# Kernel optimization log

Measured on AMD Instinct MI355X. Metric: run time of the kernel, lower is better.

Reference implementation:

```python
import jax, jax.numpy as jnp
import numpy as np


def _chamfer_min_sqdist(a, b):
    # a: [N,3], b: [M,3] -> for each point in a, min squared distance to b. [N]
    # ||a||^2 + ||b||^2 - 2 a.b^T ; clamp tiny negatives from cancellation.
    a2 = jnp.sum(a * a, axis=-1)            # [N]
    b2 = jnp.sum(b * b, axis=-1)            # [M]
    cross = a @ b.T                          # [N,M] GEMM, K=3
    d = a2[:, None] + b2[None, :] - 2.0 * cross
    return jnp.maximum(jnp.min(d, axis=1), 0.0)


def setup_inputs() -> dict:
    key = jax.random.key(0)
    k1, k2 = jax.random.split(key)
    N = 16384
    state_x = jax.random.normal(k1, (N, 3), dtype=jnp.float32)
    target = jax.random.normal(k2, (N, 3), dtype=jnp.float32)
    return {"state_x": state_x, "target": target}


def reference(state_x, target):
    # dist1: target -> nearest in state_x ; dist2: state_x -> nearest in target
    dist1 = _chamfer_min_sqdist(target, state_x)   # [N]
    dist2 = _chamfer_min_sqdist(state_x, target)   # [N]
    loss = (jnp.mean(jnp.sqrt(dist1)) + jnp.mean(jnp.sqrt(dist2))) * 0.5
    return loss * 10.0
```

## Files before the change

kernel.cpp:

```cpp
#include <hip/hip_runtime.h>
#include <math.h>


typedef __attribute__((ext_vector_type(8)))  short bf16x8;
typedef __attribute__((ext_vector_type(16))) float f32x16;

#define S_SLICES 16

__device__ __forceinline__ unsigned enc_f32(float f) {
    int b = __float_as_int(f);
    return (b >= 0) ? ((unsigned)b | 0x80000000u) : ~(unsigned)b;
}
__device__ __forceinline__ float dec_f32(unsigned k) {
    int b = (k & 0x80000000u) ? (int)(k & 0x7FFFFFFFu) : ~(int)k;
    return __int_as_float(b);
}

__device__ __forceinline__ unsigned short f2bf(float v) {
    unsigned u = __float_as_uint(v);
    u += 0x7FFFu + ((u >> 16) & 1u);
    return (unsigned short)(u >> 16);
}
__device__ __forceinline__ float bf2f(unsigned short b) {
    unsigned u = ((unsigned)b) << 16;
    return __uint_as_float(u);
}
__device__ __forceinline__ unsigned pk2(unsigned short lo, unsigned short hi) {
    return (unsigned)lo | ((unsigned)hi << 16);
}

__global__ __launch_bounds__(256) void chamfer_prep(
    const float* __restrict__ state_x, const float* __restrict__ target,
    uint4* __restrict__ AfragS, uint4* __restrict__ AfragT,
    uint4* __restrict__ BfragS, uint4* __restrict__ BfragT,
    unsigned* __restrict__ mins_u, float* __restrict__ out, int N)
{
    const int p = blockIdx.x * 256 + threadIdx.x;
    const float* src = (p < N) ? state_x : target;
    const int i = (p < N) ? p : p - N;

    const float x = src[3*i+0], y = src[3*i+1], z = src[3*i+2];
    const float n2 = fmaf(x, x, fmaf(y, y, z * z));

    const unsigned short hx = f2bf(x), hy = f2bf(y), hz = f2bf(z);
    const unsigned short lx = f2bf(x - bf2f(hx));
    const unsigned short ly = f2bf(y - bf2f(hy));
    const unsigned short lz = f2bf(z - bf2f(hz));
    const unsigned short mhx = f2bf(-2.0f*x), mhy = f2bf(-2.0f*y), mhz = f2bf(-2.0f*z);
    const unsigned short mlx = f2bf(-2.0f*x - bf2f(mhx));
    const unsigned short mly = f2bf(-2.0f*y - bf2f(mhy));
    const unsigned short mlz = f2bf(-2.0f*z - bf2f(mhz));
    const unsigned short hn = f2bf(n2);
    const unsigned short ln = f2bf(n2 - bf2f(hn));
    const unsigned short ONE = 0x3F80;

    uint4 A0 = make_uint4(pk2(mhx,mhy), pk2(mhz,mlx), pk2(mly,mlz), pk2(mhx,mhy));
    uint4 A1 = make_uint4(pk2(mhz,mlx), pk2(mly,mlz), pk2(hn,ln),   pk2(ONE,ONE));
    uint4 B0 = make_uint4(pk2(hx,hy), pk2(hz,hx), pk2(hy,hz), pk2(lx,ly));
    uint4 B1 = make_uint4(pk2(lz,lx), pk2(ly,lz), pk2(ONE,ONE), pk2(hn,ln));

    uint4* Aarr = (p < N) ? AfragS : AfragT;
    uint4* Barr = (p < N) ? BfragS : BfragT;
    Aarr[2*i+0] = A0;  Aarr[2*i+1] = A1;
    Barr[2*i+0] = B0;  Barr[2*i+1] = B1;

    mins_u[p] = 0xFFFFFFFFu;
    if (p == 0) *out = 0.0f;
}

__global__ __launch_bounds__(256) void chamfer_main(
    const bf16x8* __restrict__ AfragS, const bf16x8* __restrict__ AfragT,
    const bf16x8* __restrict__ BfragS, const bf16x8* __restrict__ BfragT,
    unsigned* __restrict__ mins_u, int N, int S)
{
    const int tid  = threadIdx.x;
    const int lane = tid & 63;
    const int l31  = lane & 31;
    const int half = lane >> 5;
    const int w    = tid >> 6;

    const int bs = blockIdx.x / S;
    const int s  = blockIdx.x % S;
    const int qblk = bs * 256;

    const bf16x8* afr;
    const bf16x8* bfr;
    if (qblk < N) { afr = AfragT + (size_t)qblk * 2;       bfr = BfragS; }
    else          { afr = AfragS + (size_t)(qblk - N) * 2; bfr = BfragT; }

    const int C = N / S;

    __shared__ uint4 ldsB[2048];
    {
        const uint4* src = (const uint4*)bfr + (size_t)(s * C) * 2;
        #pragma unroll
        for (int j = 0; j < 8; ++j)
            ldsB[tid + j * 256] = src[tid + j * 256];
    }
    __syncthreads();
    const bf16x8* lb = (const bf16x8*)ldsB;

    const int r0 = w * 64;
    const bf16x8 av0 = afr[(r0 +      l31) * 2 + half];
    const bf16x8 av1 = afr[(r0 + 32 + l31) * 2 + half];

    const int boff = l31 * 2 + half;

    f32x16 racc0, racc1, zc;
    #pragma unroll
    for (int i = 0; i < 16; ++i) { racc0[i] = 3.0e38f; racc1[i] = 3.0e38f; zc[i] = 0.0f; }

    #pragma unroll 2
    for (int it = 0; it < C / 64; ++it) {
        const bf16x8 b0 = lb[it * 128 + boff];
        const bf16x8 b1 = lb[it * 128 + 64 + boff];
        {
            f32x16 a0 = __builtin_amdgcn_mfma_f32_32x32x16_bf16(av0, b0, zc, 0, 0, 0);
            f32x16 a1 = __builtin_amdgcn_mfma_f32_32x32x16_bf16(av0, b1, zc, 0, 0, 0);
            #pragma unroll
            for (int i = 0; i < 16; ++i)
                racc0[i] = fminf(fminf(racc0[i], a0[i]), a1[i]);
        }
        {
            f32x16 a0 = __builtin_amdgcn_mfma_f32_32x32x16_bf16(av1, b0, zc, 0, 0, 0);
            f32x16 a1 = __builtin_amdgcn_mfma_f32_32x32x16_bf16(av1, b1, zc, 0, 0, 0);
            #pragma unroll
            for (int i = 0; i < 16; ++i)
                racc1[i] = fminf(fminf(racc1[i], a0[i]), a1[i]);
        }
    }

    #pragma unroll
    for (int i = 0; i < 16; ++i) {
        float v0 = racc0[i], v1 = racc1[i];
        v0 = fminf(v0, __shfl_xor(v0, 16, 64));
        v1 = fminf(v1, __shfl_xor(v1, 16, 64));
        v0 = fminf(v0, __shfl_xor(v0,  8, 64));
        v1 = fminf(v1, __shfl_xor(v1,  8, 64));
        v0 = fminf(v0, __shfl_xor(v0,  4, 64));
        v1 = fminf(v1, __shfl_xor(v1,  4, 64));
        v0 = fminf(v0, __shfl_xor(v0,  2, 64));
        v1 = fminf(v1, __shfl_xor(v1,  2, 64));
        v0 = fminf(v0, __shfl_xor(v0,  1, 64));
        v1 = fminf(v1, __shfl_xor(v1,  1, 64));
        racc0[i] = v0;
        racc1[i] = v1;
    }

    if (l31 == 0) {
        const int base = qblk + r0;
        #pragma unroll
        for (int i = 0; i < 16; ++i) {
            const int row = (i & 3) + 8 * (i >> 2) + 4 * half;
            atomicMin(&mins_u[base + row],      enc_f32(racc0[i]));
            atomicMin(&mins_u[base + 32 + row], enc_f32(racc1[i]));
        }
    }
}

__global__ __launch_bounds__(256) void chamfer_finish(
    const unsigned* __restrict__ mins_u, float* __restrict__ out, int N)
{
    const int tid = threadIdx.x;
    const int qi = blockIdx.x * 256 + tid;

    float v = sqrtf(fmaxf(dec_f32(mins_u[qi]), 0.0f));

    for (int off = 32; off > 0; off >>= 1) v += __shfl_down(v, off, 64);
    __shared__ float wsum[4];
    if ((tid & 63) == 0) wsum[tid >> 6] = v;
    __syncthreads();
    if (tid == 0) {
        const float bsum = wsum[0] + wsum[1] + wsum[2] + wsum[3];
        atomicAdd(out, bsum * 5.0f / (float)N);
    }
}

extern "C" void kernel_launch(void* const* d_in, const int* in_sizes, int n_in,
                              void* d_out, int out_size, void* d_ws, size_t ws_size,
                              hipStream_t stream)
{
    const float* state_x = (const float*)d_in[0];
    const float* target  = (const float*)d_in[1];
    float* out = (float*)d_out;

    const int N = in_sizes[0] / 3;
    const int twoN = 2 * N;

    int S = S_SLICES;
    while (S > 1 && (N % (S * 64)) != 0) S >>= 1;

    char* wsb = (char*)d_ws;
    unsigned* mins_u = (unsigned*)wsb;
    uint4* AfragS = (uint4*)(wsb + (size_t)twoN * 4);
    uint4* AfragT = (uint4*)(wsb + (size_t)twoN * 4 + (size_t)N * 32);
    uint4* BfragS = (uint4*)(wsb + (size_t)twoN * 4 + (size_t)N * 64);
    uint4* BfragT = (uint4*)(wsb + (size_t)twoN * 4 + (size_t)N * 96);

    chamfer_prep<<<twoN / 256, 256, 0, stream>>>(
        state_x, target, AfragS, AfragT, BfragS, BfragT, mins_u, out, N);

    const int rowBlocks = twoN / 256;
    chamfer_main<<<rowBlocks * S, 256, 0, stream>>>(
        (const bf16x8*)AfragS, (const bf16x8*)AfragT,
        (const bf16x8*)BfragS, (const bf16x8*)BfragT, mins_u, N, S);

    chamfer_finish<<<twoN / 256, 256, 0, stream>>>(mins_u, out, N);
}
```

Baseline: 94.61 us.

## Reorder B fragments for contiguous LDS reads, batch MFMAs, LDS row-min reduction

The prep kernel now writes B fragments in a per-64-point tiled order, so each half-wave reads a contiguous run of LDS and avoids the strided pattern. The main loop issues all four MFMAs through inline asm and then pads with a fixed s_nop before the min updates, which removes compiler interleaving. The final cross-lane shuffle reduction and the 32 atomics per lane group are replaced by an XOR-swizzled LDS transpose, after which each thread reduces one row and does a single atomicMin. The inline asm bypasses compiler hazard tracking, so the manual nop must be enough for correctness.

```diff
diff --git a/kernel.cpp b/kernel.cpp
--- a/kernel.cpp
+++ b/kernel.cpp
@@ -27,6 +27,13 @@
 }
 __device__ __forceinline__ unsigned pk2(unsigned short lo, unsigned short hi) {
     return (unsigned)lo | ((unsigned)hi << 16);
+}
+
+__device__ __forceinline__ f32x16 mfma_v(bf16x8 a, bf16x8 b, f32x16 c) {
+    f32x16 d;
+    asm("v_mfma_f32_32x32x16_bf16 %0, %1, %2, %3"
+        : "=&v"(d) : "v"(a), "v"(b), "v"(c));
+    return d;
 }
 
 __global__ __launch_bounds__(256) void chamfer_prep(
@@ -62,7 +69,10 @@
     uint4* Aarr = (p < N) ? AfragS : AfragT;
     uint4* Barr = (p < N) ? BfragS : BfragT;
     Aarr[2*i+0] = A0;  Aarr[2*i+1] = A1;
-    Barr[2*i+0] = B0;  Barr[2*i+1] = B1;
+
+    const int bbase = (i >> 6) * 128 + ((i >> 5) & 1) * 64 + (i & 31);
+    Barr[bbase +  0] = B0;
+    Barr[bbase + 32] = B1;
 
     mins_u[p] = 0xFFFFFFFFu;
     if (p == 0) *out = 0.0f;
@@ -104,7 +114,7 @@
     const bf16x8 av0 = afr[(r0 +      l31) * 2 + half];
     const bf16x8 av1 = afr[(r0 + 32 + l31) * 2 + half];
 
-    const int boff = l31 * 2 + half;
+    const int boff = half * 32 + l31;
 
     f32x16 racc0, racc1, zc;
     #pragma unroll
@@ -114,47 +124,46 @@
     for (int it = 0; it < C / 64; ++it) {
         const bf16x8 b0 = lb[it * 128 + boff];
         const bf16x8 b1 = lb[it * 128 + 64 + boff];
-        {
-            f32x16 a0 = __builtin_amdgcn_mfma_f32_32x32x16_bf16(av0, b0, zc, 0, 0, 0);
-            f32x16 a1 = __builtin_amdgcn_mfma_f32_32x32x16_bf16(av0, b1, zc, 0, 0, 0);
-            #pragma unroll
-            for (int i = 0; i < 16; ++i)
-                racc0[i] = fminf(fminf(racc0[i], a0[i]), a1[i]);
-        }
-        {
-            f32x16 a0 = __builtin_amdgcn_mfma_f32_32x32x16_bf16(av1, b0, zc, 0, 0, 0);
-            f32x16 a1 = __builtin_amdgcn_mfma_f32_32x32x16_bf16(av1, b1, zc, 0, 0, 0);
-            #pragma unroll
-            for (int i = 0; i < 16; ++i)
-                racc1[i] = fminf(fminf(racc1[i], a0[i]), a1[i]);
-        }
-    }
-
+        f32x16 a0 = mfma_v(av0, b0, zc);
+        f32x16 a1 = mfma_v(av0, b1, zc);
+        f32x16 a2 = mfma_v(av1, b0, zc);
+        f32x16 a3 = mfma_v(av1, b1, zc);
+        __builtin_amdgcn_sched_barrier(0);
+        asm volatile("s_nop 7");
+        __builtin_amdgcn_sched_barrier(0);
+        #pragma unroll
+        for (int i = 0; i < 16; ++i)
+            racc0[i] = fminf(fminf(racc0[i], a0[i]), a1[i]);
+        #pragma unroll
+        for (int i = 0; i < 16; ++i)
+            racc1[i] = fminf(fminf(racc1[i], a2[i]), a3[i]);
+    }
+
+    __syncthreads();
+    float* lf = (float*)ldsB;
+    const int cg = l31 >> 2, cl = l31 & 3;
     #pragma unroll
     for (int i = 0; i < 16; ++i) {
-        float v0 = racc0[i], v1 = racc1[i];
-        v0 = fminf(v0, __shfl_xor(v0, 16, 64));
-        v1 = fminf(v1, __shfl_xor(v1, 16, 64));
-        v0 = fminf(v0, __shfl_xor(v0,  8, 64));
-        v1 = fminf(v1, __shfl_xor(v1,  8, 64));
-        v0 = fminf(v0, __shfl_xor(v0,  4, 64));
-        v1 = fminf(v1, __shfl_xor(v1,  4, 64));
-        v0 = fminf(v0, __shfl_xor(v0,  2, 64));
-        v1 = fminf(v1, __shfl_xor(v1,  2, 64));
-        v0 = fminf(v0, __shfl_xor(v0,  1, 64));
-        v1 = fminf(v1, __shfl_xor(v1,  1, 64));
-        racc0[i] = v0;
-        racc1[i] = v1;
-    }
-
-    if (l31 == 0) {
-        const int base = qblk + r0;
-        #pragma unroll
-        for (int i = 0; i < 16; ++i) {
-            const int row = (i & 3) + 8 * (i >> 2) + 4 * half;
-            atomicMin(&mins_u[base + row],      enc_f32(racc0[i]));
-            atomicMin(&mins_u[base + 32 + row], enc_f32(racc1[i]));
+        const int row0 = (i & 3) + 8 * (i >> 2) + 4 * half;
+        const int row1 = row0 + 32;
+        lf[w * 2048 + row0 * 32 + ((cg ^ (row0 & 7)) << 2) + cl] = racc0[i];
+        lf[w * 2048 + row1 * 32 + ((cg ^ (row1 & 7)) << 2) + cl] = racc1[i];
+    }
+    __syncthreads();
+    {
+        const int r = tid & 63, wr = tid >> 6;
+        const float4* rowp = (const float4*)(lf + wr * 2048 + r * 32);
+        float m0 = 3.0e38f, m1 = 3.0e38f;
+        #pragma unroll
+        for (int g = 0; g < 8; g += 2) {
+            const float4 v0 = rowp[g ^ (r & 7)];
+            const float4 v1 = rowp[(g + 1) ^ (r & 7)];
+            m0 = fminf(fminf(m0, v0.x), fminf(v0.y, v0.z));
+            m0 = fminf(m0, v0.w);
+            m1 = fminf(fminf(m1, v1.x), fminf(v1.y, v1.z));
+            m1 = fminf(m1, v1.w);
         }
+        atomicMin(&mins_u[qblk + wr * 64 + r], enc_f32(fminf(m0, m1)));
     }
 }
 
```

Result: faster. 79.94 us (-15.5%).
